# Optimization experiments

Hardware: AMD Instinct MI355X
Metric: run time of the kernel (lower is better)

Reference implementation:

```python
import jax, jax.numpy as jnp
import numpy as np

FIR_LO = {
    'db4': np.array([-0.0105974017850021, 0.0328830116668852, 0.0308413818355607, -0.1870348117188811,
                     -0.0279837694169839, 0.6308807679295904, 0.7148465705529155, 0.2303778133088964], np.float32),
    'db6': np.array([0.00107730108499558, -0.00477725751101065, -0.0005538422009938, 0.03158203931748603,
                     0.02752286553030533, -0.0975016055873225, -0.12976686756709563, 0.22626469396544,
                     0.3152503517092432, -0.7511339080210959, 0.4946238903984534, 0.1115407433501095], np.float32),
    'sym6': np.array([-0.007800708325034148, 0.001767711864242804, 0.04472490177066578, -0.02106029251230056,
                      -0.0726375227866, 0.3379294217282401, 0.787641141030194, 0.4910559419267466,
                      -0.048311742585632, -0.1179901111484105, 0.00349071208421747, 0.01540410932702737], np.float32),
    'coif5': np.array([-3.459977283621256e-05, -7.098330313814114e-05, 0.0004662169601128863, 0.001117518770890601,
                       -0.002574517688750223, -0.00900797613666158, 0.015880544863615904, 0.03455502757306163,
                       -0.08230192710688598, -0.07179982161931202, 0.42848347637761874, 0.7937772226256206,
                       0.4051769024096169, -0.06112339000267287, -0.06577191128185562, 0.023452696141836267,
                       0.007782596427325418, -0.003793512864491014, -0.0002606761356811993, 0.000107502882505652,
                       1.10319778524429e-05, -5.520763127949e-06, -1.0682196848076e-06, 5.236425333584e-07,
                       1.125098976034e-07, -5.417490769329e-08, -8.8631e-09, 4.2921e-09, 6.7e-10, -3.2e-10], np.float32),
}

CANDIDATES = ['db4', 'db6', 'sym6', 'coif5', 'bior53', 'bior97']
LIFT_53 = [(-0.5, True), (0.25, False)]
LIFT_97 = [(-1.586134342, True), (-0.05298011854, False), (0.8829110762, True), (0.4435068522, False)]


def _pad_reflect(x, hpad, wpad):
    if hpad == (0, 0) and wpad == (0, 0):
        return x
    return jnp.pad(x, ((0, 0), (0, 0), hpad, wpad), mode='reflect')


def _lo(name):
    lo = jnp.asarray(FIR_LO[name])
    return lo / (jnp.sqrt(jnp.sum(lo * lo)) + 1e-12)


def _hi_from_lo(lo):
    L = lo.shape[0]
    sign = jnp.cos(jnp.pi * jnp.arange(L, dtype=lo.dtype))  # (-1)^n
    return sign * lo[::-1]


def _sep_conv(x, k, dim):
    # x: (N,1,H,W); k: (L,) 1D filter applied separably along dim (cross-correlation, stride 1)
    L = k.shape[0]
    pl = (L - 1) // 2
    pa, pb = ((pl - 1, pl) if L % 2 == 0 else (pl, pl))
    if dim == 'W':
        xp = _pad_reflect(x, (0, 0), (pa, pb))
        kern = k.reshape(1, 1, 1, L)
    else:
        xp = _pad_reflect(x, (pa, pb), (0, 0))
        kern = k.reshape(1, 1, L, 1)
    return jax.lax.conv_general_dilated(xp, kern, (1, 1), 'VALID',
                                        dimension_numbers=('NCHW', 'OIHW', 'NCHW'))


def _split_even_odd(x, dim):
    if dim == 'W':
        if x.shape[3] % 2 == 1:
            x = _pad_reflect(x, (0, 0), (0, 1))
        return x[..., 0::2], x[..., 1::2]
    if x.shape[2] % 2 == 1:
        x = _pad_reflect(x, (0, 1), (0, 0))
    return x[..., 0::2, :], x[..., 1::2, :]


def _nb_sum(x, dim):
    # 0.5*(left+right) with reflect padding == conv with kernel [0.5, 0, 0.5]
    if dim == 'W':
        xp = _pad_reflect(x, (0, 0), (1, 1))
        return 0.5 * (xp[..., :-2] + xp[..., 2:])
    xp = _pad_reflect(x, (1, 1), (0, 0))
    return 0.5 * (xp[..., :-2, :] + xp[..., 2:, :])


def _lift(x, dim, steps, sA, sD):
    even, odd = _split_even_odd(x, dim)
    for coeff, is_pred in steps:
        if is_pred:
            odd = odd + coeff * _nb_sum(even, dim)
        else:
            even = even + coeff * _nb_sum(odd, dim)
    return sA * even, sD * odd


def _one_level_1d(x, cand, dim, p):
    if cand == 'bior53':
        return _lift(x, dim, LIFT_53, p['s53A'], p['s53D'])
    if cand == 'bior97':
        return _lift(x, dim, LIFT_97, p['s97A'], p['s97D'])
    lo = _lo(cand)
    return _sep_conv(x, lo, dim), _sep_conv(x, _hi_from_lo(lo), dim)


def _one_level_2d(x, cand, p):
    H, W = x.shape[2], x.shape[3]
    Lw, Hw = _one_level_1d(x, cand, 'W', p)
    LL, LH = _one_level_1d(Lw, cand, 'H', p)
    HL, HH = _one_level_1d(Hw, cand, 'H', p)

    def up(t):
        if t.shape[2] == H and t.shape[3] == W:
            return t
        return jax.image.resize(t, (t.shape[0], t.shape[1], H, W), method='bilinear')  # align_corners=False

    hf = p['hf']
    return up(LL), up(LH) * hf, up(HL) * hf, up(HH) * hf


def reference(x, gate_w1, gate_b1, gate_w2, gate_b2, scale53_A, scale53_D,
              scale97_A, scale97_D, hf_scale, proj_w, proj_b):
    B, C, H, W = x.shape
    # gate: 1x1 conv -> relu -> 1x1 conv -> softmax over K candidates
    h = jax.nn.relu(jnp.einsum('bchw,oc->bohw', x, gate_w1) + gate_b1[None, :, None, None])
    logits = jnp.einsum('bchw,oc->bohw', h, gate_w2) + gate_b2[None, :, None, None]
    gate_w = jax.nn.softmax(logits, axis=1)  # (B,K,H,W)

    x_bc = x.reshape(B * C, 1, H, W)
    p = {'s53A': scale53_A, 's53D': scale53_D, 's97A': scale97_A, 's97D': scale97_D, 'hf': hf_scale}
    bands = [_one_level_2d(x_bc, c, p) for c in CANDIDATES]
    # stack over K candidates -> (B*C, K, H, W) per subband
    LL = jnp.concatenate([b[0] for b in bands], axis=1)
    LH = jnp.concatenate([b[1] for b in bands], axis=1)
    HL = jnp.concatenate([b[2] for b in bands], axis=1)
    HH = jnp.concatenate([b[3] for b in bands], axis=1)

    w = jnp.repeat(gate_w, C, axis=0)  # (B*C,K,H,W), same as repeat_interleave on batch
    w = w / (jnp.sum(w, axis=1, keepdims=True) + 1e-12)
    LL_f = jnp.sum(LL * w, axis=1)
    LH_f = jnp.sum(LH * w, axis=1)
    HL_f = jnp.sum(HL * w, axis=1)
    HH_f = jnp.sum(HH * w, axis=1)

    Y = jnp.stack([LL_f, LH_f, HL_f, HH_f], axis=1).reshape(B, C * 4, H, W)
    return jnp.einsum('bchw,oc->bohw', Y, proj_w) + proj_b[None, :, None, None]


def setup_inputs() -> dict:
    key = jax.random.key(0)
    ks = jax.random.split(key, 5)
    C, hidden, K, Cout = 32, 8, 6, 32
    return {
        'x': jax.random.normal(ks[0], (4, C, 192, 192), jnp.float32),
        'gate_w1': jax.random.normal(ks[1], (hidden, C), jnp.float32) * (1.0 / np.sqrt(C)),
        'gate_b1': jnp.zeros((hidden,), jnp.float32),
        'gate_w2': jax.random.normal(ks[2], (K, hidden), jnp.float32) * (1.0 / np.sqrt(hidden)),
        'gate_b2': jnp.zeros((K,), jnp.float32),
        'scale53_A': jnp.float32(1.0),
        'scale53_D': jnp.float32(1.0),
        'scale97_A': jnp.float32(1.149604398),
        'scale97_D': jnp.float32(1.0 / 1.149604398),
        'hf_scale': jnp.float32(0.9),
        'proj_w': jax.random.normal(ks[3], (Cout, 4 * C), jnp.float32) * (1.0 / np.sqrt(4 * C)),
        'proj_b': jnp.zeros((Cout,), jnp.float32),
    }
```

## Files before the change

kernel.cpp:

```cpp
#include <hip/hip_runtime.h>
#include <hip/hip_fp16.h>

#define HW 36864
#define IMGS 128

typedef _Float16 h16;
typedef _Float16 v8h __attribute__((ext_vector_type(8)));
typedef _Float16 v4h __attribute__((ext_vector_type(4)));
typedef float v4f __attribute__((ext_vector_type(4)));

static __device__ __forceinline__ int imax(int a, int b) { return a > b ? a : b; }
static __device__ __forceinline__ int imin(int a, int b) { return a < b ? a : b; }

__device__ __constant__ float LIFT_C[6] = {
  -0.5f, 0.25f,
  -1.586134342f, -0.05298011854f, 0.8829110762f, 0.4435068522f
};
__device__ __constant__ int FIR_L[4]   = {8, 12, 12, 30};
__device__ __constant__ int FIR_PA[4]  = {2, 4, 4, 13};
__device__ __constant__ int FIR_OFF[4] = {0, 8, 20, 32};

__device__ constexpr float FIRC[62] = {
  -0.0105974017850021f, 0.0328830116668852f, 0.0308413818355607f, -0.1870348117188811f,
  -0.0279837694169839f, 0.6308807679295904f, 0.7148465705529155f, 0.2303778133088964f,
  0.00107730108499558f, -0.00477725751101065f, -0.0005538422009938f, 0.03158203931748603f,
  0.02752286553030533f, -0.0975016055873225f, -0.12976686756709563f, 0.22626469396544f,
  0.3152503517092432f, -0.7511339080210959f, 0.4946238903984534f, 0.1115407433501095f,
  -0.007800708325034148f, 0.001767711864242804f, 0.04472490177066578f, -0.02106029251230056f,
  -0.0726375227866f, 0.3379294217282401f, 0.787641141030194f, 0.4910559419267466f,
  -0.048311742585632f, -0.1179901111484105f, 0.00349071208421747f, 0.01540410932702737f,
  -3.459977283621256e-05f, -7.098330313814114e-05f, 0.0004662169601128863f, 0.001117518770890601f,
  -0.002574517688750223f, -0.00900797613666158f, 0.015880544863615904f, 0.03455502757306163f,
  -0.08230192710688598f, -0.07179982161931202f, 0.42848347637761874f, 0.7937772226256206f,
  0.4051769024096169f, -0.06112339000267287f, -0.06577191128185562f, 0.023452696141836267f,
  0.007782596427325418f, -0.003793512864491014f, -0.0002606761356811993f, 0.000107502882505652f,
  1.10319778524429e-05f, -5.520763127949e-06f, -1.0682196848076e-06f, 5.236425333584e-07f,
  1.125098976034e-07f, -5.417490769329e-08f, -8.8631e-09f, 4.2921e-09f, 6.7e-10f, -3.2e-10f,
};

__global__ __launch_bounds__(256) void k_gate(
    const float* __restrict__ x, const float* __restrict__ w1, const float* __restrict__ b1,
    const float* __restrict__ w2, const float* __restrict__ b2, h16* __restrict__ gate)
{
  __shared__ float w1s[256], b1s[8], w2s[48], b2s[6];
  int tid = threadIdx.x;
  w1s[tid] = w1[tid];
  if (tid < 8)  b1s[tid] = b1[tid];
  if (tid < 48) w2s[tid] = w2[tid];
  if (tid < 6)  b2s[tid] = b2[tid];
  __syncthreads();
  int px = blockIdx.x * 256 + tid;
  int b = px / HW, p = px - b * HW;
  const float* xb = x + (size_t)b * 32 * HW + p;
  float xv[32];
#pragma unroll
  for (int c = 0; c < 32; ++c) xv[c] = xb[(size_t)c * HW];
  float hb[8];
#pragma unroll
  for (int j = 0; j < 8; ++j) {
    float s = b1s[j];
#pragma unroll
    for (int c = 0; c < 32; ++c) s += w1s[j * 32 + c] * xv[c];
    hb[j] = fmaxf(s, 0.f);
  }
  float e[6], mx = -1e30f;
#pragma unroll
  for (int k = 0; k < 6; ++k) {
    float s = b2s[k];
#pragma unroll
    for (int j = 0; j < 8; ++j) s += w2s[k * 8 + j] * hb[j];
    e[k] = s; mx = fmaxf(mx, s);
  }
  float se = 0.f;
#pragma unroll
  for (int k = 0; k < 6; ++k) { e[k] = expf(e[k] - mx); se += e[k]; }
  float inv = 1.f / se, s2 = 0.f;
#pragma unroll
  for (int k = 0; k < 6; ++k) { e[k] *= inv; s2 += e[k]; }
  float inv2 = 1.f / (s2 + 1e-12f);
  h16* gp = gate + (size_t)b * 6 * HW + p;
#pragma unroll
  for (int k = 0; k < 6; ++k) gp[(size_t)k * HW] = (h16)(e[k] * inv2);
}

__global__ __launch_bounds__(64) void k_build(
    h16* __restrict__ Kall, const float* __restrict__ s53A, const float* __restrict__ s53D,
    const float* __restrict__ s97A, const float* __restrict__ s97D)
{
  const int col = blockIdx.x;
  const int mat = blockIdx.y;
  const int cand = mat >> 1, side = mat & 1;
  const int tid = threadIdx.x;
  h16* out = Kall + (size_t)mat * HW;
  if (cand < 4) {
    const int Lf = FIR_L[cand], PA = FIR_PA[cand], OFF = FIR_OFF[cand];
    float ss = 0.f;
    for (int j = 0; j < Lf; ++j) ss += FIRC[OFF + j] * FIRC[OFF + j];
    const float invn = 1.f / (sqrtf(ss) + 1e-12f);
    for (int i = tid; i < 192; i += 64) {
      const int d = (i < 96) ? 1 : 2;
      const int q0 = i - d;
      const int i0 = imax(q0, 0), i1 = imin(q0 + 1, 189);
      const float tt = (float)d - (float)(2 * i + 1) * (1.f / 192.f);
      float c0 = 0.f, c1 = 0.f;
      for (int j = 0; j < Lf; ++j) {
        float fj = side ? (((j & 1) ? -1.f : 1.f) * FIRC[OFF + Lf - 1 - j]) : FIRC[OFF + j];
        fj *= invn;
        int r0 = i0 + j - PA; r0 = r0 < 0 ? -r0 : (r0 > 191 ? 382 - r0 : r0);
        int r1 = i1 + j - PA; r1 = r1 < 0 ? -r1 : (r1 > 191 ? 382 - r1 : r1);
        if (r0 == col) c0 += fj;
        if (r1 == col) c1 += fj;
      }
      out[(size_t)i * 192 + col] = (h16)((1.f - tt) * c0 + tt * c1);
    }
  } else {
    __shared__ float yb[192];
    __shared__ float sb[96];
    yb[tid] = 0.f; yb[tid + 64] = 0.f; yb[tid + 128] = 0.f;
    __syncthreads();
    if (tid == 0) yb[col] = 1.f;
    __syncthreads();
    const int c97 = (cand == 5);
    const int base = c97 ? 2 : 0, ns = c97 ? 4 : 2;
    for (int s = 0; s < ns; ++s) {
      const float cf = LIFT_C[base + s] * 0.5f;
      for (int j = tid; j < 96; j += 64) {
        int jm = (j == 0) ? 1 : j - 1, jp = (j == 95) ? 94 : j + 1;
        if ((s & 1) == 0) yb[2 * j + 1] += cf * (yb[2 * jm] + yb[2 * jp]);
        else              yb[2 * j]     += cf * (yb[2 * jm + 1] + yb[2 * jp + 1]);
      }
      __syncthreads();
    }
    const float sA = c97 ? s97A[0] : s53A[0];
    const float sD = c97 ? s97D[0] : s53D[0];
    for (int u = tid; u < 96; u += 64)
      sb[u] = side ? sD * yb[2 * u + 1] : sA * yb[2 * u];
    __syncthreads();
    for (int i = tid; i < 192; i += 64) {
      const int u0 = (i >> 1) + (i & 1) - 1;
      const float tt = (i & 1) ? 0.25f : 0.75f;
      const int a0 = imax(u0, 0), a1 = imin(u0 + 1, 95);
      out[(size_t)i * 192 + col] = (h16)((1.f - tt) * sb[a0] + tt * sb[a1]);
    }
  }
}

__global__ __launch_bounds__(768, 2) void k_gw(
    const float* __restrict__ x, const h16* __restrict__ Kall, h16* __restrict__ P)
{
  __shared__ h16 As[96 * 200];
  const int half = blockIdx.x & 1, pg = blockIdx.x >> 1;
  const int img  = blockIdx.y;
  const int tid = threadIdx.x;
  const float* xi = x + (size_t)img * HW + (size_t)half * 96 * 192;
  for (int u = tid; u < 2304; u += 768) {
    int r = u / 24, c8 = u - r * 24;
    float4 v0 = *(const float4*)(xi + (size_t)r * 192 + c8 * 8);
    float4 v1 = *(const float4*)(xi + (size_t)r * 192 + c8 * 8 + 4);
    v8h h;
    h[0] = (h16)v0.x; h[1] = (h16)v0.y; h[2] = (h16)v0.z; h[3] = (h16)v0.w;
    h[4] = (h16)v1.x; h[5] = (h16)v1.y; h[6] = (h16)v1.z; h[7] = (h16)v1.w;
    *(v8h*)(As + (size_t)r * 200 + c8 * 8) = h;
  }
  __syncthreads();
  const int lane = tid & 63, wv = tid >> 6;
  const int lm = lane & 15, quad = lane >> 4;
  const int mt = wv >> 1, nh = wv & 1;
  const int mrow = mt * 16;
  const int hg = half * 96 + mrow + quad * 4;
#pragma unroll
  for (int pl = 0; pl < 3; ++pl) {
    const int plane = pg * 3 + pl;
    const h16* KB = Kall + (size_t)plane * HW;
    h16* Pp = P + ((size_t)plane * IMGS + img) * HW;
#pragma unroll
    for (int t6 = 0; t6 < 6; ++t6) {
      const int n0 = (nh * 6 + t6) * 16;
      int kt0 = (n0 - 24) >> 5; kt0 = kt0 < 0 ? 0 : (kt0 > 3 ? 3 : kt0);
      v4f C = (v4f){0.f, 0.f, 0.f, 0.f};
#pragma unroll
      for (int kt = 0; kt < 3; ++kt) {
        const int k0 = (kt0 + kt) * 32 + quad * 8;
        v8h a = *(const v8h*)(As + (size_t)(mrow + lm) * 200 + k0);
        v8h b = *(const v8h*)(KB + (size_t)(n0 + lm) * 192 + k0);
        C = __builtin_amdgcn_mfma_f32_16x16x32_f16(a, b, C, 0, 0, 0);
      }
      const int q = n0 / 48;
      const int wq = n0 - q * 48 + lm;
      v4h o;
      o[0] = (h16)C[0]; o[1] = (h16)C[1]; o[2] = (h16)C[2]; o[3] = (h16)C[3];
      *(v4h*)(Pp + (size_t)q * 9216 + (size_t)wq * 192 + hg) = o;
    }
  }
}

__global__ __launch_bounds__(256, 2) void k_gh2(
    const h16* __restrict__ Kall, const h16* __restrict__ P, const h16* __restrict__ gate,
    const float* __restrict__ hfp, h16* __restrict__ sf)
{
  __shared__ h16 Bs[48 * 200];
  const int bx = blockIdx.x;
  const int sw = bx & 1, qt = (bx >> 1) & 3, mh = bx >> 3;
  const int img = blockIdx.y;
  const int bimg = img >> 5;
  const int tid = threadIdx.x;
  const int lane = tid & 63, wv = tid >> 6;
  const int lm = lane & 15, quad = lane >> 4;
  const int sh = wv & 1, w4h = wv >> 1;
  const int w0q = qt * 48;
  const int mbase = mh * 96 + w4h * 48;

  const int wp0 = tid / 24,           c80 = tid - wp0 * 24;
  const int it1 = tid + 256;  const int wp1 = it1 / 24, c81 = it1 - wp1 * 24;
  const int it2 = tid + 512;  const int wp2 = it2 / 24, c82 = it2 - wp2 * 24;
  const int it3 = tid + 768;  const int wp3 = it3 / 24, c83 = it3 - wp3 * 24;
  const int it4 = tid + 1024; const int wp4 = it4 / 24, c84 = it4 - wp4 * 24;

  v4f acc[3][3];
#pragma unroll
  for (int mi = 0; mi < 3; ++mi)
#pragma unroll
    for (int nt = 0; nt < 3; ++nt) acc[mi][nt] = (v4f){0.f, 0.f, 0.f, 0.f};

  const h16* Ps = P + ((size_t)sw * IMGS + img) * HW + (size_t)qt * 9216;
  v8h p0 = *(const v8h*)(Ps + (size_t)wp0 * 192 + c80 * 8);
  v8h p1 = *(const v8h*)(Ps + (size_t)wp1 * 192 + c81 * 8);
  v8h p2 = *(const v8h*)(Ps + (size_t)wp2 * 192 + c82 * 8);
  v8h p3 = *(const v8h*)(Ps + (size_t)wp3 * 192 + c83 * 8);
  v8h p4;
  if (tid < 128) p4 = *(const v8h*)(Ps + (size_t)wp4 * 192 + c84 * 8);

  for (int cand = 0; cand < 6; ++cand) {
    *(v8h*)(Bs + (size_t)wp0 * 200 + c80 * 8) = p0;
    *(v8h*)(Bs + (size_t)wp1 * 200 + c81 * 8) = p1;
    *(v8h*)(Bs + (size_t)wp2 * 200 + c82 * 8) = p2;
    *(v8h*)(Bs + (size_t)wp3 * 200 + c83 * 8) = p3;
    if (tid < 128) *(v8h*)(Bs + (size_t)wp4 * 200 + c84 * 8) = p4;
    __syncthreads();
    if (cand < 5) {
      const h16* Pn = P + ((size_t)((cand + 1) * 2 + sw) * IMGS + img) * HW + (size_t)qt * 9216;
      p0 = *(const v8h*)(Pn + (size_t)wp0 * 192 + c80 * 8);
      p1 = *(const v8h*)(Pn + (size_t)wp1 * 192 + c81 * 8);
      p2 = *(const v8h*)(Pn + (size_t)wp2 * 192 + c82 * 8);
      p3 = *(const v8h*)(Pn + (size_t)wp3 * 192 + c83 * 8);
      if (tid < 128) p4 = *(const v8h*)(Pn + (size_t)wp4 * 192 + c84 * 8);
    }
    const h16* g16 = gate + (size_t)(bimg * 6 + cand) * HW;
    const h16* KB = Kall + (size_t)(cand * 2 + sh) * HW;
#pragma unroll
    for (int mi = 0; mi < 3; ++mi) {
      const int m0 = mbase + mi * 16;
      const int ktlo = imax(0, (m0 - 24) >> 5), kthi = imin(5, (m0 + 39) >> 5);
      const int hr0 = m0 + quad * 4;
      float g[3][4];
#pragma unroll
      for (int nt = 0; nt < 3; ++nt)
#pragma unroll
        for (int r = 0; r < 4; ++r)
          g[nt][r] = (float)g16[(size_t)(hr0 + r) * 192 + w0q + nt * 16 + lm];
      v4f C[3];
#pragma unroll
      for (int nt = 0; nt < 3; ++nt) C[nt] = (v4f){0.f, 0.f, 0.f, 0.f};
      for (int kt = ktlo; kt <= kthi; ++kt) {
        const int k0 = kt * 32 + quad * 8;
        v8h a = *(const v8h*)(KB + (size_t)(m0 + lm) * 192 + k0);
#pragma unroll
        for (int nt = 0; nt < 3; ++nt) {
          v8h b = *(const v8h*)(Bs + (size_t)(nt * 16 + lm) * 200 + k0);
          C[nt] = __builtin_amdgcn_mfma_f32_16x16x32_f16(a, b, C[nt], 0, 0, 0);
        }
      }
#pragma unroll
      for (int nt = 0; nt < 3; ++nt)
#pragma unroll
        for (int r = 0; r < 4; ++r)
          acc[mi][nt][r] += g[nt][r] * C[nt][r];
    }
    __syncthreads();
  }
  const float hfv = hfp[0];
  const int s = sw * 2 + sh;
  const float f = (s == 0) ? 1.f : hfv;
  h16* Op = sf + ((size_t)img * 4 + s) * HW;
#pragma unroll
  for (int mi = 0; mi < 3; ++mi) {
    const int hr0 = mbase + mi * 16 + quad * 4;
#pragma unroll
    for (int nt = 0; nt < 3; ++nt) {
      const int wc = w0q + nt * 16 + lm;
#pragma unroll
      for (int r = 0; r < 4; ++r)
        Op[(size_t)(hr0 + r) * 192 + wc] = (h16)(f * acc[mi][nt][r]);
    }
  }
}

__global__ __launch_bounds__(256) void k_proj(
    const h16* __restrict__ sf, const float* __restrict__ pw,
    const float* __restrict__ pb, float* __restrict__ out)
{
  const int tid = threadIdx.x;
  const int lane = tid & 63;
  const int og = __builtin_amdgcn_readfirstlane(tid >> 6);
  const int b = blockIdx.x / 144;
  const int p = (blockIdx.x - b * 144) * 256 + lane * 4;
  const h16* sfb = sf + (size_t)(b * 128) * HW + p;
  const float* pwb = pw + og * 8 * 128;
  float acc[8][4];
#pragma unroll
  for (int oo = 0; oo < 8; ++oo)
#pragma unroll
    for (int j = 0; j < 4; ++j) acc[oo][j] = 0.f;
#pragma unroll 4
  for (int ch = 0; ch < 128; ++ch) {
    v4h hv = *(const v4h*)(sfb + (size_t)ch * HW);
    float v[4];
#pragma unroll
    for (int j = 0; j < 4; ++j) v[j] = (float)hv[j];
#pragma unroll
    for (int oo = 0; oo < 8; ++oo) {
      const float w = pwb[oo * 128 + ch];
#pragma unroll
      for (int j = 0; j < 4; ++j) acc[oo][j] = fmaf(w, v[j], acc[oo][j]);
    }
  }
#pragma unroll
  for (int oo = 0; oo < 8; ++oo) {
    const float bb = pb[og * 8 + oo];
    float4 o4;
    o4.x = acc[oo][0] + bb; o4.y = acc[oo][1] + bb;
    o4.z = acc[oo][2] + bb; o4.w = acc[oo][3] + bb;
    *(float4*)(out + (size_t)(b * 32 + og * 8 + oo) * HW + p) = o4;
  }
}

extern "C" void kernel_launch(void* const* d_in, const int* in_sizes, int n_in,
                              void* d_out, int out_size, void* d_ws, size_t ws_size,
                              hipStream_t stream) {
  (void)in_sizes; (void)n_in; (void)out_size; (void)ws_size;
  const float* x    = (const float*)d_in[0];
  const float* gw1  = (const float*)d_in[1];
  const float* gb1  = (const float*)d_in[2];
  const float* gw2  = (const float*)d_in[3];
  const float* gb2  = (const float*)d_in[4];
  const float* s53A = (const float*)d_in[5];
  const float* s53D = (const float*)d_in[6];
  const float* s97A = (const float*)d_in[7];
  const float* s97D = (const float*)d_in[8];
  const float* hfp  = (const float*)d_in[9];
  const float* pw   = (const float*)d_in[10];
  const float* pb   = (const float*)d_in[11];
  float* out = (float*)d_out;

  h16* gate = (h16*)d_ws;
  h16* Kall = (h16*)((char*)d_ws + 1769472);
  h16* P    = (h16*)((char*)d_ws + 2654208);
  h16* sf   = (h16*)((char*)d_ws + 115900416);

  hipLaunchKernelGGL(k_gate, dim3(576), dim3(256), 0, stream, x, gw1, gb1, gw2, gb2, gate);
  hipLaunchKernelGGL(k_build, dim3(192, 12), dim3(64), 0, stream, Kall, s53A, s53D, s97A, s97D);
  hipLaunchKernelGGL(k_gw, dim3(8, IMGS), dim3(768), 0, stream, x, Kall, P);
  hipLaunchKernelGGL(k_gh2, dim3(16, IMGS), dim3(256), 0, stream, Kall, P, gate, hfp, sf);
  hipLaunchKernelGGL(k_proj, dim3(576), dim3(256), 0, stream, sf, pw, pb, out);
}
```

Before: 313.4 us.

## Restructure width-GEMM kernel into single-wave blocks reusing x fragments across planes

The k_gw kernel changes from 768-thread blocks that stage a half image in LDS to 64-thread single-wave blocks. Each wave loads its x fragments straight from global memory into registers, then loops over all 12 filter planes, reusing those fragments for the MFMAs. This removes the LDS staging and the barrier and cuts how often x is reloaded across planes. The trade-offs are higher register pressure and output stores that are now scalar and strided, which may hurt write coalescing.

After: 277.1 us. 1.13x faster.

```diff
diff --git a/kernel.cpp b/kernel.cpp
--- a/kernel.cpp
+++ b/kernel.cpp
@@ -145,52 +145,54 @@
   }
 }
 
-__global__ __launch_bounds__(768, 2) void k_gw(
+__global__ __launch_bounds__(64) void k_gw(
     const float* __restrict__ x, const h16* __restrict__ Kall, h16* __restrict__ P)
 {
-  __shared__ h16 As[96 * 200];
-  const int half = blockIdx.x & 1, pg = blockIdx.x >> 1;
-  const int img  = blockIdx.y;
-  const int tid = threadIdx.x;
-  const float* xi = x + (size_t)img * HW + (size_t)half * 96 * 192;
-  for (int u = tid; u < 2304; u += 768) {
-    int r = u / 24, c8 = u - r * 24;
-    float4 v0 = *(const float4*)(xi + (size_t)r * 192 + c8 * 8);
-    float4 v1 = *(const float4*)(xi + (size_t)r * 192 + c8 * 8 + 4);
-    v8h h;
-    h[0] = (h16)v0.x; h[1] = (h16)v0.y; h[2] = (h16)v0.z; h[3] = (h16)v0.w;
-    h[4] = (h16)v1.x; h[5] = (h16)v1.y; h[6] = (h16)v1.z; h[7] = (h16)v1.w;
-    *(v8h*)(As + (size_t)r * 200 + c8 * 8) = h;
-  }
-  __syncthreads();
-  const int lane = tid & 63, wv = tid >> 6;
+  const int bx = blockIdx.x;
+  const int mt = bx % 12, hc = bx / 12;
+  const int img = blockIdx.y;
+  const int lane = threadIdx.x;
   const int lm = lane & 15, quad = lane >> 4;
-  const int mt = wv >> 1, nh = wv & 1;
-  const int mrow = mt * 16;
-  const int hg = half * 96 + mrow + quad * 4;
-#pragma unroll
-  for (int pl = 0; pl < 3; ++pl) {
-    const int plane = pg * 3 + pl;
-    const h16* KB = Kall + (size_t)plane * HW;
-    h16* Pp = P + ((size_t)plane * IMGS + img) * HW;
-#pragma unroll
-    for (int t6 = 0; t6 < 6; ++t6) {
-      const int n0 = (nh * 6 + t6) * 16;
-      int kt0 = (n0 - 24) >> 5; kt0 = kt0 < 0 ? 0 : (kt0 > 3 ? 3 : kt0);
-      v4f C = (v4f){0.f, 0.f, 0.f, 0.f};
-#pragma unroll
-      for (int kt = 0; kt < 3; ++kt) {
-        const int k0 = (kt0 + kt) * 32 + quad * 8;
-        v8h a = *(const v8h*)(As + (size_t)(mrow + lm) * 200 + k0);
-        v8h b = *(const v8h*)(KB + (size_t)(n0 + lm) * 192 + k0);
-        C = __builtin_amdgcn_mfma_f32_16x16x32_f16(a, b, C, 0, 0, 0);
-      }
-      const int q = n0 / 48;
-      const int wq = n0 - q * 48 + lm;
-      v4h o;
-      o[0] = (h16)C[0]; o[1] = (h16)C[1]; o[2] = (h16)C[2]; o[3] = (h16)C[3];
-      *(v4h*)(Pp + (size_t)q * 9216 + (size_t)wq * 192 + hg) = o;
-    }
+  const int m0 = mt * 16;
+  int ktr = (m0 - 24) >> 5; ktr = ktr < 0 ? 0 : (ktr > 3 ? 3 : ktr);
+  const int q = mt / 3;
+  const int wqb = m0 - q * 48;
+  const float* xi = x + (size_t)img * HW;
+
+  v8h b[4][3];
+#pragma unroll
+  for (int j = 0; j < 4; ++j)
+#pragma unroll
+    for (int kt = 0; kt < 3; ++kt) {
+      const float* xr = xi + (size_t)(hc * 64 + j * 16 + lm) * 192 + (ktr + kt) * 32 + quad * 8;
+      float4 u0 = *(const float4*)xr;
+      float4 u1 = *(const float4*)(xr + 4);
+      v8h t;
+      t[0] = (h16)u0.x; t[1] = (h16)u0.y; t[2] = (h16)u0.z; t[3] = (h16)u0.w;
+      t[4] = (h16)u1.x; t[5] = (h16)u1.y; t[6] = (h16)u1.z; t[7] = (h16)u1.w;
+      b[j][kt] = t;
+    }
+#pragma unroll 2
+  for (int plane = 0; plane < 12; ++plane) {
+    const h16* KW = Kall + (size_t)plane * HW + (size_t)(m0 + lm) * 192 + ktr * 32 + quad * 8;
+    v8h a0 = *(const v8h*)(KW);
+    v8h a1 = *(const v8h*)(KW + 32);
+    v8h a2 = *(const v8h*)(KW + 64);
+    v4f C[4];
+#pragma unroll
+    for (int j = 0; j < 4; ++j) C[j] = (v4f){0.f, 0.f, 0.f, 0.f};
+#pragma unroll
+    for (int j = 0; j < 4; ++j) {
+      C[j] = __builtin_amdgcn_mfma_f32_16x16x32_f16(a0, b[j][0], C[j], 0, 0, 0);
+      C[j] = __builtin_amdgcn_mfma_f32_16x16x32_f16(a1, b[j][1], C[j], 0, 0, 0);
+      C[j] = __builtin_amdgcn_mfma_f32_16x16x32_f16(a2, b[j][2], C[j], 0, 0, 0);
+    }
+    h16* Pp = P + ((size_t)plane * IMGS + img) * HW + (size_t)q * 9216;
+#pragma unroll
+    for (int j = 0; j < 4; ++j)
+#pragma unroll
+      for (int r = 0; r < 4; ++r)
+        Pp[(size_t)(wqb + quad * 4 + r) * 192 + hc * 64 + j * 16 + lm] = (h16)C[j][r];
   }
 }
 
@@ -359,7 +361,7 @@
 
   hipLaunchKernelGGL(k_gate, dim3(576), dim3(256), 0, stream, x, gw1, gb1, gw2, gb2, gate);
   hipLaunchKernelGGL(k_build, dim3(192, 12), dim3(64), 0, stream, Kall, s53A, s53D, s97A, s97D);
-  hipLaunchKernelGGL(k_gw, dim3(8, IMGS), dim3(768), 0, stream, x, Kall, P);
+  hipLaunchKernelGGL(k_gw, dim3(36, IMGS), dim3(64), 0, stream, x, Kall, P);
   hipLaunchKernelGGL(k_gh2, dim3(16, IMGS), dim3(256), 0, stream, Kall, P, gate, hfp, sf);
   hipLaunchKernelGGL(k_proj, dim3(576), dim3(256), 0, stream, sf, pw, pb, out);
 }
```
